# Kernel optimization log

Hardware: AMD Instinct MI355X
Metric: run time of the kernel (lower is better)

## Reference

```python
import jax, jax.numpy as jnp
import numpy as np

B, T, C, H = 2, 2048, 1024, 16
HS = C // H  # 64
EPS = 1e-5


def layer_norm(x, w, b):
    mu = jnp.mean(x, axis=-1, keepdims=True)
    var = jnp.var(x, axis=-1, keepdims=True)
    return (x - mu) * jax.lax.rsqrt(var + EPS) * w + b


def setup_inputs() -> dict:
    key = jax.random.key(0)
    ks = jax.random.split(key, 16)
    s_c = 1.0 / np.sqrt(C)
    s_f = 1.0 / np.sqrt(4 * C)
    u = lambda k, shape, s: jax.random.uniform(k, shape, jnp.float32, -s, s)
    return {
        "x": jax.random.normal(ks[0], (B, T, C), jnp.float32),
        # per-head Q/K/V Linears stacked over heads: [H, C, HS], bias [H, HS]
        "Wq": u(ks[1], (H, C, HS), s_c), "bq": u(ks[2], (H, HS), s_c),
        "Wk": u(ks[3], (H, C, HS), s_c), "bk": u(ks[4], (H, HS), s_c),
        "Wv": u(ks[5], (H, C, HS), s_c), "bv": u(ks[6], (H, HS), s_c),
        "Wp": u(ks[7], (C, C), s_c), "bp": u(ks[8], (C,), s_c),
        "W1": u(ks[9], (C, 4 * C), s_c), "b1": u(ks[10], (4 * C,), s_c),
        "W2": u(ks[11], (4 * C, C), s_f), "b2": u(ks[12], (C,), s_f),
        "ln1_w": jnp.ones((C,), jnp.float32), "ln1_b": jnp.zeros((C,), jnp.float32),
        "ln2_w": jnp.ones((C,), jnp.float32), "ln2_b": jnp.zeros((C,), jnp.float32),
    }


def reference(x, Wq, bq, Wk, bk, Wv, bv, Wp, bp, W1, b1, W2, b2,
              ln1_w, ln1_b, ln2_w, ln2_b):
    # --- pre-norm self-attention ---
    xn = layer_norm(x, ln1_w, ln1_b)
    q = jnp.einsum('btc,hcd->bhtd', xn, Wq) + bq[None, :, None, :]
    k = jnp.einsum('btc,hcd->bhtd', xn, Wk) + bk[None, :, None, :]
    v = jnp.einsum('btc,hcd->bhtd', xn, Wv) + bv[None, :, None, :]
    # NOTE: original scales by C**-0.5 (full embedding dim), not head_size**-0.5
    att = jnp.einsum('bhtd,bhsd->bhts', q, k) * (C ** -0.5)
    att = jax.nn.softmax(att, axis=-1)
    o = jnp.einsum('bhts,bhsd->bhtd', att, v)  # [B,H,T,HS]
    o = jnp.transpose(o, (0, 2, 1, 3)).reshape(B, T, C)  # concat heads
    sa = o @ Wp + bp
    out = x + sa
    # --- pre-norm FFN (exact erf GELU, matching nn.GELU default) ---
    on = layer_norm(out, ln2_w, ln2_b)
    h = jax.nn.gelu(on @ W1 + b1, approximate=False)
    return out + (h @ W2 + b2)
```

## Files before the change

### kernel.cpp

```cpp
#include <hip/hip_runtime.h>
#include <math.h>

#define BB 2
#define TT 2048
#define CC 1024
#define HH 16
#define HS 64
#define MT 4096
#define FF 4096

typedef unsigned short u16;
typedef __bf16 bfrag __attribute__((ext_vector_type(8)));
typedef float f4 __attribute__((ext_vector_type(4)));

#define AS1(p) ((const __attribute__((address_space(1))) void*)(p))
#define AS3(p) ((__attribute__((address_space(3))) void*)(p))

__device__ __forceinline__ u16 f2bf(float f) {
  union { float f; unsigned u; } a; a.f = f;
  return (u16)((a.u + 0x7fffu + ((a.u >> 16) & 1u)) >> 16);
}

__device__ __forceinline__ int swz128(int byteoff) {
  return byteoff ^ (((byteoff >> 7) & 7) << 4);
}

__global__ void tr_f32_bf16(const float* __restrict__ src, u16* __restrict__ dst,
                            int R, int Cc, long long sb, long long db, int dld) {
  __shared__ float t[32][33];
  const int bz = blockIdx.z;
  const int r0 = blockIdx.y * 32, c0 = blockIdx.x * 32;
  const int tx = threadIdx.x, ty = threadIdx.y;
  const float* s = src + bz * sb;
  u16* d = dst + bz * db;
#pragma unroll
  for (int i = 0; i < 4; i++)
    t[ty + i * 8][tx] = s[(size_t)(r0 + ty + i * 8) * Cc + c0 + tx];
  __syncthreads();
#pragma unroll
  for (int i = 0; i < 4; i++)
    d[(size_t)(c0 + ty + i * 8) * dld + r0 + tx] = f2bf(t[tx][ty + i * 8]);
}

__global__ void tr_bf16(const u16* __restrict__ src, u16* __restrict__ dst,
                        int R, int Cc, long long sb, long long db, int dld) {
  __shared__ u16 t[32][33];
  const int bz = blockIdx.z;
  const int r0 = blockIdx.y * 32, c0 = blockIdx.x * 32;
  const int tx = threadIdx.x, ty = threadIdx.y;
  const u16* s = src + bz * sb;
  u16* d = dst + bz * db;
#pragma unroll
  for (int i = 0; i < 4; i++)
    t[ty + i * 8][tx] = s[(size_t)(r0 + ty + i * 8) * Cc + c0 + tx];
  __syncthreads();
#pragma unroll
  for (int i = 0; i < 4; i++)
    d[(size_t)(c0 + ty + i * 8) * dld + r0 + tx] = t[tx][ty + i * 8];
}

__global__ __launch_bounds__(256) void ln_kernel(
    const float* __restrict__ x, const float* __restrict__ w,
    const float* __restrict__ b, u16* __restrict__ y) {
  const int row = blockIdx.x, tid = threadIdx.x;
  const float4 v = reinterpret_cast<const float4*>(x + (size_t)row * CC)[tid];
  float s = v.x + v.y + v.z + v.w;
  float s2 = v.x * v.x + v.y * v.y + v.z * v.z + v.w * v.w;
#pragma unroll
  for (int off = 32; off >= 1; off >>= 1) {
    s += __shfl_xor(s, off);
    s2 += __shfl_xor(s2, off);
  }
  __shared__ float ps[4], ps2[4];
  const int wave = tid >> 6, lane = tid & 63;
  if (lane == 0) { ps[wave] = s; ps2[wave] = s2; }
  __syncthreads();
  s = ps[0] + ps[1] + ps[2] + ps[3];
  s2 = ps2[0] + ps2[1] + ps2[2] + ps2[3];
  const float mu = s * (1.f / CC);
  const float rstd = rsqrtf(s2 * (1.f / CC) - mu * mu + 1e-5f);
  const float4 wv = reinterpret_cast<const float4*>(w)[tid];
  const float4 bv = reinterpret_cast<const float4*>(b)[tid];
  ushort4 o;
  o.x = f2bf((v.x - mu) * rstd * wv.x + bv.x);
  o.y = f2bf((v.y - mu) * rstd * wv.y + bv.y);
  o.z = f2bf((v.z - mu) * rstd * wv.z + bv.z);
  o.w = f2bf((v.w - mu) * rstd * wv.w + bv.w);
  reinterpret_cast<ushort4*>(y + (size_t)row * CC)[tid] = o;
}

__device__ __forceinline__ void gemm128_core(
    const u16* __restrict__ A, const u16* __restrict__ Bt, int K,
    f4 (&acc)[4][4]) {
  __shared__ u16 As[128 * 32];
  __shared__ u16 Bs[128 * 32];
  const int tid = threadIdx.x;
  const int wave = tid >> 6, lane = tid & 63;
  const int wm = wave >> 1, wn = wave & 1;
  const int lg = lane >> 4, ll = lane & 15;

  const u16* ga = A + (size_t)(blockIdx.y * 128 + (tid >> 2)) * K + (tid & 3) * 8;
  const u16* gb = Bt + (size_t)(blockIdx.x * 128 + (tid >> 2)) * K + (tid & 3) * 8;
  u16* la = As + tid * 8;
  u16* lb = Bs + tid * 8;
  const size_t g64 = (size_t)64 * K;

  for (int kt = 0; kt < K; kt += 32) {
    __builtin_amdgcn_global_load_lds(AS1(ga), AS3(la), 16, 0, 0);
    __builtin_amdgcn_global_load_lds(AS1(ga + g64), AS3(la + 2048), 16, 0, 0);
    __builtin_amdgcn_global_load_lds(AS1(gb), AS3(lb), 16, 0, 0);
    __builtin_amdgcn_global_load_lds(AS1(gb + g64), AS3(lb + 2048), 16, 0, 0);
    __syncthreads();
    bfrag af[4], bf[4];
#pragma unroll
    for (int i = 0; i < 4; i++) {
      af[i] = *(const bfrag*)&As[(wm * 64 + i * 16 + ll) * 32 + lg * 8];
      bf[i] = *(const bfrag*)&Bs[(wn * 64 + i * 16 + ll) * 32 + lg * 8];
    }
#pragma unroll
    for (int i = 0; i < 4; i++)
#pragma unroll
      for (int j = 0; j < 4; j++)
        acc[i][j] = __builtin_amdgcn_mfma_f32_16x16x32_bf16(af[i], bf[j], acc[i][j], 0, 0, 0);
    __syncthreads();
    ga += 32; gb += 32;
  }
}

#define EPI_COORDS                                              \
  const int tid = threadIdx.x;                                  \
  const int wave = tid >> 6, lane = tid & 63;                   \
  const int wm = wave >> 1, wn = wave & 1;                      \
  const int lg = lane >> 4, ll = lane & 15;

__global__ __launch_bounds__(256, 2) void gemm_qkv(
    const u16* __restrict__ A, const u16* __restrict__ Bt,
    const float* __restrict__ bq, const float* __restrict__ bk,
    const float* __restrict__ bv,
    u16* __restrict__ q, u16* __restrict__ k, u16* __restrict__ v) {
  f4 acc[4][4] = {};
  gemm128_core(A, Bt, CC, acc);
  EPI_COORDS
#pragma unroll
  for (int j = 0; j < 4; j++) {
    const int n = blockIdx.x * 128 + wn * 64 + j * 16 + ll;
    const int sec = n >> 10, nn = n & 1023, h = nn >> 6, d = nn & 63;
    const float bias = (sec == 0 ? bq : (sec == 1 ? bk : bv))[nn];
    const float scale = (sec == 0) ? 0.03125f : 1.0f;
    u16* dst = sec == 0 ? q : (sec == 1 ? k : v);
#pragma unroll
    for (int i = 0; i < 4; i++)
#pragma unroll
      for (int r = 0; r < 4; r++) {
        const int m = blockIdx.y * 128 + wm * 64 + i * 16 + lg * 4 + r;
        const int b = m >> 11, t = m & 2047;
        dst[(((size_t)b * HH + h) * TT + t) * HS + d] = f2bf((acc[i][j][r] + bias) * scale);
      }
  }
}

__global__ __launch_bounds__(256, 2) void gemm_proj(
    const u16* __restrict__ A, const u16* __restrict__ Bt,
    const float* __restrict__ bp, const float* __restrict__ x,
    float* __restrict__ outw) {
  f4 acc[4][4] = {};
  gemm128_core(A, Bt, CC, acc);
  EPI_COORDS
#pragma unroll
  for (int i = 0; i < 4; i++)
#pragma unroll
    for (int j = 0; j < 4; j++) {
      const int n = blockIdx.x * 128 + wn * 64 + j * 16 + ll;
      const float bias = bp[n];
#pragma unroll
      for (int r = 0; r < 4; r++) {
        const int m = blockIdx.y * 128 + wm * 64 + i * 16 + lg * 4 + r;
        const size_t idx = (size_t)m * CC + n;
        outw[idx] = acc[i][j][r] + bias + x[idx];
      }
    }
}

__global__ __launch_bounds__(256, 2) void gemm_ffn1(
    const u16* __restrict__ A, const u16* __restrict__ Bt,
    const float* __restrict__ b1, u16* __restrict__ hb) {
  f4 acc[4][4] = {};
  gemm128_core(A, Bt, CC, acc);
  EPI_COORDS
#pragma unroll
  for (int i = 0; i < 4; i++)
#pragma unroll
    for (int j = 0; j < 4; j++) {
      const int n = blockIdx.x * 128 + wn * 64 + j * 16 + ll;
      const float bias = b1[n];
#pragma unroll
      for (int r = 0; r < 4; r++) {
        const int m = blockIdx.y * 128 + wm * 64 + i * 16 + lg * 4 + r;
        const float t = acc[i][j][r] + bias;
        const float g = 0.5f * t * (1.0f + erff(t * 0.70710678118654752f));
        hb[(size_t)m * FF + n] = f2bf(g);
      }
    }
}

__global__ __launch_bounds__(256, 2) void gemm_ffn2(
    const u16* __restrict__ A, const u16* __restrict__ Bt,
    const float* __restrict__ b2, const float* __restrict__ outw,
    float* __restrict__ dout) {
  f4 acc[4][4] = {};
  gemm128_core(A, Bt, FF, acc);
  EPI_COORDS
#pragma unroll
  for (int i = 0; i < 4; i++)
#pragma unroll
    for (int j = 0; j < 4; j++) {
      const int n = blockIdx.x * 128 + wn * 64 + j * 16 + ll;
      const float bias = b2[n];
#pragma unroll
      for (int r = 0; r < 4; r++) {
        const int m = blockIdx.y * 128 + wm * 64 + i * 16 + lg * 4 + r;
        const size_t idx = (size_t)m * CC + n;
        dout[idx] = acc[i][j][r] + bias + outw[idx];
      }
    }
}

__global__ __launch_bounds__(256, 2) void attn_kernel(
    const u16* __restrict__ Q, const u16* __restrict__ Kb,
    const u16* __restrict__ Vt, u16* __restrict__ Ao) {
  __shared__ __align__(1024) u16 Ks[2][64 * 64];
  __shared__ __align__(1024) u16 Vs[2][64 * 64];
  __shared__ __align__(1024) u16 Ps[4][32 * 64];
  const int bh = blockIdx.y, qt = blockIdx.x;
  const int tid = threadIdx.x, wave = tid >> 6, lane = tid & 63;
  const int lg = lane >> 4, ll = lane & 15;

  bfrag qf[2][2];
  const u16* Qb = Q + ((size_t)bh * TT + qt * 128 + wave * 32) * HS;
#pragma unroll
  for (int qb = 0; qb < 2; qb++)
#pragma unroll
    for (int dc = 0; dc < 2; dc++)
      qf[qb][dc] = *(const bfrag*)&Qb[(qb * 16 + ll) * HS + dc * 32 + lg * 8];

  f4 o[2][4] = {};
  float mrun[2] = {-INFINITY, -INFINITY}, lrun[2] = {0.f, 0.f};

  const int trow = tid >> 3;
  const int tch  = (tid & 7) ^ (trow & 7);
  const u16* gk = Kb + ((size_t)bh * TT + trow) * HS + tch * 8;
  const u16* gv = Vt + ((size_t)bh * HS + trow) * TT + tch * 8;

  char* const pw = (char*)Ps[wave];

#define STAGE(bufi, stt)                                                          \
  do {                                                                            \
    u16* lk = &Ks[bufi][tid * 8];                                                 \
    u16* lv = &Vs[bufi][tid * 8];                                                 \
    __builtin_amdgcn_global_load_lds(AS1(gk + (size_t)(stt) * HS), AS3(lk), 16, 0, 0); \
    __builtin_amdgcn_global_load_lds(AS1(gk + (size_t)(stt) * HS + 32 * HS), AS3(lk + 2048), 16, 0, 0); \
    __builtin_amdgcn_global_load_lds(AS1(gv + (stt)), AS3(lv), 16, 0, 0);         \
    __builtin_amdgcn_global_load_lds(AS1(gv + (stt) + (size_t)32 * TT), AS3(lv + 2048), 16, 0, 0); \
  } while (0)

  STAGE(0, 0);
  int cur = 0;

  for (int st = 0; st < TT; st += 64) {
    if (st + 64 < TT) {
      STAGE(cur ^ 1, st + 64);
      asm volatile("s_waitcnt vmcnt(4)" ::: "memory");
    } else {
      asm volatile("s_waitcnt vmcnt(0)" ::: "memory");
    }
    __builtin_amdgcn_s_barrier();
    __builtin_amdgcn_sched_barrier(0);

    const char* kbuf = (const char*)Ks[cur];
    const char* vbuf = (const char*)Vs[cur];

    f4 p[2][4];
#pragma unroll
    for (int kb = 0; kb < 4; kb++) {
      const int row = kb * 16 + ll;
      const bfrag k0 = *(const bfrag*)(kbuf + swz128(row * 128 + lg * 16));
      const bfrag k1 = *(const bfrag*)(kbuf + swz128(row * 128 + 64 + lg * 16));
#pragma unroll
      for (int qb = 0; qb < 2; qb++) {
        f4 z = {0.f, 0.f, 0.f, 0.f};
        z = __builtin_amdgcn_mfma_f32_16x16x32_bf16(k0, qf[qb][0], z, 0, 0, 0);
        p[qb][kb] = __builtin_amdgcn_mfma_f32_16x16x32_bf16(k1, qf[qb][1], z, 0, 0, 0);
      }
    }

#pragma unroll
    for (int qb = 0; qb < 2; qb++) {
      float pm = p[qb][0][0];
#pragma unroll
      for (int kb = 0; kb < 4; kb++)
#pragma unroll
        for (int r = 0; r < 4; r++)
          if (kb | r) pm = fmaxf(pm, p[qb][kb][r]);
      pm = fmaxf(pm, __shfl_xor(pm, 16));
      pm = fmaxf(pm, __shfl_xor(pm, 32));
      const float mn = fmaxf(mrun[qb], pm);
      const float al = __expf(mrun[qb] - mn);
      mrun[qb] = mn;
      float rs = 0.f;
#pragma unroll
      for (int kb = 0; kb < 4; kb++)
#pragma unroll
        for (int r = 0; r < 4; r++) {
          const float e = __expf(p[qb][kb][r] - mn);
          p[qb][kb][r] = e;
          rs += e;
        }
      rs += __shfl_xor(rs, 16);
      rs += __shfl_xor(rs, 32);
      lrun[qb] = lrun[qb] * al + rs;
#pragma unroll
      for (int fo = 0; fo < 4; fo++) o[qb][fo] *= al;
#pragma unroll
      for (int kb = 0; kb < 4; kb++) {
        union { uint2 v; __bf16 h[4]; } w;
        w.h[0] = (__bf16)p[qb][kb][0];
        w.h[1] = (__bf16)p[qb][kb][1];
        w.h[2] = (__bf16)p[qb][kb][2];
        w.h[3] = (__bf16)p[qb][kb][3];
        *(uint2*)(pw + swz128((qb * 16 + ll) * 128 + kb * 32 + lg * 8)) = w.v;
      }
    }

#pragma unroll
    for (int ks = 0; ks < 2; ks++) {
      const bfrag pb0 = *(const bfrag*)(pw + swz128(ll * 128 + ks * 64 + lg * 16));
      const bfrag pb1 = *(const bfrag*)(pw + swz128((16 + ll) * 128 + ks * 64 + lg * 16));
#pragma unroll
      for (int fo = 0; fo < 4; fo++) {
        const bfrag vf = *(const bfrag*)(vbuf + swz128((fo * 16 + ll) * 128 + ks * 64 + lg * 16));
        o[0][fo] = __builtin_amdgcn_mfma_f32_16x16x32_bf16(vf, pb0, o[0][fo], 0, 0, 0);
        o[1][fo] = __builtin_amdgcn_mfma_f32_16x16x32_bf16(vf, pb1, o[1][fo], 0, 0, 0);
      }
    }

    __builtin_amdgcn_sched_barrier(0);
    __builtin_amdgcn_s_barrier();
    cur ^= 1;
  }
#undef STAGE

  const int b = bh >> 4, h = bh & 15;
#pragma unroll
  for (int qb = 0; qb < 2; qb++) {
    const float inv = 1.0f / lrun[qb];
    const int t = qt * 128 + wave * 32 + qb * 16 + ll;
#pragma unroll
    for (int fo = 0; fo < 4; fo++) {
      union { uint2 v; __bf16 h[4]; } w;
      w.h[0] = (__bf16)(o[qb][fo][0] * inv);
      w.h[1] = (__bf16)(o[qb][fo][1] * inv);
      w.h[2] = (__bf16)(o[qb][fo][2] * inv);
      w.h[3] = (__bf16)(o[qb][fo][3] * inv);
      *(uint2*)&Ao[((size_t)b * TT + t) * CC + h * HS + fo * 16 + lg * 4] = w.v;
    }
  }
}

extern "C" void kernel_launch(void* const* d_in, const int* in_sizes, int n_in,
                              void* d_out, int out_size, void* d_ws, size_t ws_size,
                              hipStream_t stream) {
  const float* x    = (const float*)d_in[0];
  const float* Wq   = (const float*)d_in[1];
  const float* bq   = (const float*)d_in[2];
  const float* Wk   = (const float*)d_in[3];
  const float* bk   = (const float*)d_in[4];
  const float* Wv   = (const float*)d_in[5];
  const float* bv   = (const float*)d_in[6];
  const float* Wp   = (const float*)d_in[7];
  const float* bp   = (const float*)d_in[8];
  const float* W1   = (const float*)d_in[9];
  const float* b1   = (const float*)d_in[10];
  const float* W2   = (const float*)d_in[11];
  const float* b2   = (const float*)d_in[12];
  const float* ln1w = (const float*)d_in[13];
  const float* ln1b = (const float*)d_in[14];
  const float* ln2w = (const float*)d_in[15];
  const float* ln2b = (const float*)d_in[16];
  float* dout = (float*)d_out;

  char* ws = (char*)d_ws;
  u16* wqkv = (u16*)(ws + 0);
  u16* wpt  = (u16*)(ws + 6291456);
  u16* w1t  = (u16*)(ws + 8388608);
  u16* w2t  = (u16*)(ws + 16777216);
  u16* xn   = (u16*)(ws + 25165824);
  u16* qb   = (u16*)(ws + 33554432);
  u16* kb   = (u16*)(ws + 41943040);
  u16* vb   = (u16*)(ws + 50331648);
  u16* vt   = (u16*)(ws + 58720256);
  u16* ao   = (u16*)(ws + 67108864);
  u16* hb   = qb;

  dim3 blk256(256);
  dim3 blkT(32, 8);

  tr_f32_bf16<<<dim3(2, 32, 16), blkT, 0, stream>>>(Wq, wqkv,               1024,   64, 65536LL, 65536LL, 1024);
  tr_f32_bf16<<<dim3(2, 32, 16), blkT, 0, stream>>>(Wk, wqkv + 1024 * 1024, 1024,   64, 65536LL, 65536LL, 1024);
  tr_f32_bf16<<<dim3(2, 32, 16), blkT, 0, stream>>>(Wv, wqkv + 2048 * 1024, 1024,   64, 65536LL, 65536LL, 1024);
  tr_f32_bf16<<<dim3(32, 32, 1),  blkT, 0, stream>>>(Wp, wpt, 1024, 1024, 0LL, 0LL, 1024);
  tr_f32_bf16<<<dim3(128, 32, 1), blkT, 0, stream>>>(W1, w1t, 1024, 4096, 0LL, 0LL, 1024);
  tr_f32_bf16<<<dim3(32, 128, 1), blkT, 0, stream>>>(W2, w2t, 4096, 1024, 0LL, 0LL, 4096);

  ln_kernel<<<dim3(MT), blk256, 0, stream>>>(x, ln1w, ln1b, xn);

  gemm_qkv<<<dim3(24, 32), blk256, 0, stream>>>(xn, wqkv, bq, bk, bv, qb, kb, vb);

  tr_bf16<<<dim3(2, 64, 32), blkT, 0, stream>>>(vb, vt, 2048, 64, 131072LL, 131072LL, 2048);

  attn_kernel<<<dim3(16, 32), blk256, 0, stream>>>(qb, kb, vt, ao);

  gemm_proj<<<dim3(8, 32), blk256, 0, stream>>>(ao, wpt, bp, x, dout);

  ln_kernel<<<dim3(MT), blk256, 0, stream>>>(dout, ln2w, ln2b, xn);

  gemm_ffn1<<<dim3(32, 32), blk256, 0, stream>>>(xn, w1t, b1, hb);
  gemm_ffn2<<<dim3(8, 32), blk256, 0, stream>>>(hb, w2t, b2, dout, dout);
}
```

Before: 298.0 us.

## Triple-buffer GEMM core with async LDS loads, swizzle, and narrower N tiles

Rewrites the shared GEMM core to use a 3-stage LDS ring fed by global_load_lds, with explicit vmcnt waits so loads for future k-tiles overlap MFMA work. An XOR swizzle on the 16-byte chunks is applied on the load and fragment-read sides to cut LDS bank conflicts, and MFMA sections raise wave priority. The proj and FFN2 GEMMs (N=1024) switch to 128x64 tiles so they launch twice as many blocks and fill the CUs better. The trade-off is roughly 3x the LDS per block, which may lower occupancy, plus hand-tuned waitcnt counts that must match the number of issued loads.

```diff
diff --git a/kernel.cpp b/kernel.cpp
--- a/kernel.cpp
+++ b/kernel.cpp
@@ -23,6 +23,10 @@
 
 __device__ __forceinline__ int swz128(int byteoff) {
   return byteoff ^ (((byteoff >> 7) & 7) << 4);
+}
+
+__device__ __forceinline__ int swzAB(int byteoff) {
+  return byteoff ^ (((byteoff >> 7) & 3) << 4);
 }
 
 __global__ void tr_f32_bf16(const float* __restrict__ src, u16* __restrict__ dst,
@@ -89,41 +93,77 @@
   reinterpret_cast<ushort4*>(y + (size_t)row * CC)[tid] = o;
 }
 
-__device__ __forceinline__ void gemm128_core(
+template<int NJ>
+__device__ __forceinline__ void gemm_core(
     const u16* __restrict__ A, const u16* __restrict__ Bt, int K,
-    f4 (&acc)[4][4]) {
-  __shared__ u16 As[128 * 32];
-  __shared__ u16 Bs[128 * 32];
+    f4 (&acc)[4][NJ]) {
+  constexpr int BN = NJ * 32;
+  __shared__ u16 As[3][128 * 32];
+  __shared__ u16 Bs[3][BN * 32];
   const int tid = threadIdx.x;
   const int wave = tid >> 6, lane = tid & 63;
   const int wm = wave >> 1, wn = wave & 1;
   const int lg = lane >> 4, ll = lane & 15;
 
-  const u16* ga = A + (size_t)(blockIdx.y * 128 + (tid >> 2)) * K + (tid & 3) * 8;
-  const u16* gb = Bt + (size_t)(blockIdx.x * 128 + (tid >> 2)) * K + (tid & 3) * 8;
-  u16* la = As + tid * 8;
-  u16* lb = Bs + tid * 8;
+  const int trow = tid >> 2;
+  const int tch  = (tid & 3) ^ ((trow >> 1) & 3);
+  const u16* ga = A + (size_t)(blockIdx.y * 128 + trow) * K + tch * 8;
+  const u16* gb = Bt + (size_t)(blockIdx.x * BN + trow) * K + tch * 8;
   const size_t g64 = (size_t)64 * K;
-
-  for (int kt = 0; kt < K; kt += 32) {
-    __builtin_amdgcn_global_load_lds(AS1(ga), AS3(la), 16, 0, 0);
-    __builtin_amdgcn_global_load_lds(AS1(ga + g64), AS3(la + 2048), 16, 0, 0);
-    __builtin_amdgcn_global_load_lds(AS1(gb), AS3(lb), 16, 0, 0);
-    __builtin_amdgcn_global_load_lds(AS1(gb + g64), AS3(lb + 2048), 16, 0, 0);
-    __syncthreads();
-    bfrag af[4], bf[4];
-#pragma unroll
-    for (int i = 0; i < 4; i++) {
-      af[i] = *(const bfrag*)&As[(wm * 64 + i * 16 + ll) * 32 + lg * 8];
-      bf[i] = *(const bfrag*)&Bs[(wn * 64 + i * 16 + ll) * 32 + lg * 8];
-    }
+  const int nt = K >> 5;
+
+  auto GSTAGE = [&](int bi, int kt) {
+    u16* la = &As[bi][tid * 8];
+    u16* lb = &Bs[bi][tid * 8];
+    const u16* gA = ga + kt * 32;
+    const u16* gB = gb + kt * 32;
+    __builtin_amdgcn_global_load_lds(AS1(gA), AS3(la), 16, 0, 0);
+    __builtin_amdgcn_global_load_lds(AS1(gA + g64), AS3(la + 2048), 16, 0, 0);
+    __builtin_amdgcn_global_load_lds(AS1(gB), AS3(lb), 16, 0, 0);
+    if constexpr (NJ == 4)
+      __builtin_amdgcn_global_load_lds(AS1(gB + g64), AS3(lb + 2048), 16, 0, 0);
+  };
+
+  GSTAGE(0, 0);
+  GSTAGE(1, 1);
+  GSTAGE(2, 2);
+  int bi = 0;
+  for (int t = 0; t < nt; t++) {
+    const int ahead = nt - 1 - t;
+    if constexpr (NJ == 4) {
+      if (ahead >= 2)      asm volatile("s_waitcnt vmcnt(8)" ::: "memory");
+      else if (ahead == 1) asm volatile("s_waitcnt vmcnt(4)" ::: "memory");
+      else                 asm volatile("s_waitcnt vmcnt(0)" ::: "memory");
+    } else {
+      if (ahead >= 2)      asm volatile("s_waitcnt vmcnt(6)" ::: "memory");
+      else if (ahead == 1) asm volatile("s_waitcnt vmcnt(3)" ::: "memory");
+      else                 asm volatile("s_waitcnt vmcnt(0)" ::: "memory");
+    }
+    __builtin_amdgcn_s_barrier();
+    __builtin_amdgcn_sched_barrier(0);
+
+    const char* as_ = (const char*)As[bi];
+    const char* bs_ = (const char*)Bs[bi];
+    bfrag af[4], bf[NJ];
 #pragma unroll
     for (int i = 0; i < 4; i++)
-#pragma unroll
-      for (int j = 0; j < 4; j++)
+      af[i] = *(const bfrag*)(as_ + swzAB((wm * 64 + i * 16 + ll) * 64 + lg * 16));
+#pragma unroll
+    for (int j = 0; j < NJ; j++)
+      bf[j] = *(const bfrag*)(bs_ + swzAB((wn * (BN / 2) + j * 16 + ll) * 64 + lg * 16));
+
+    __builtin_amdgcn_s_setprio(1);
+#pragma unroll
+    for (int i = 0; i < 4; i++)
+#pragma unroll
+      for (int j = 0; j < NJ; j++)
         acc[i][j] = __builtin_amdgcn_mfma_f32_16x16x32_bf16(af[i], bf[j], acc[i][j], 0, 0, 0);
-    __syncthreads();
-    ga += 32; gb += 32;
+    __builtin_amdgcn_s_setprio(0);
+
+    __builtin_amdgcn_sched_barrier(0);
+    __builtin_amdgcn_s_barrier();
+    if (t + 3 < nt) GSTAGE(bi, t + 3);
+    bi = (bi == 2) ? 0 : bi + 1;
   }
 }
 
@@ -139,7 +179,7 @@
     const float* __restrict__ bv,
     u16* __restrict__ q, u16* __restrict__ k, u16* __restrict__ v) {
   f4 acc[4][4] = {};
-  gemm128_core(A, Bt, CC, acc);
+  gemm_core<4>(A, Bt, CC, acc);
   EPI_COORDS
 #pragma unroll
   for (int j = 0; j < 4; j++) {
@@ -163,14 +203,14 @@
     const u16* __restrict__ A, const u16* __restrict__ Bt,
     const float* __restrict__ bp, const float* __restrict__ x,
     float* __restrict__ outw) {
-  f4 acc[4][4] = {};
-  gemm128_core(A, Bt, CC, acc);
+  f4 acc[4][2] = {};
+  gemm_core<2>(A, Bt, CC, acc);
   EPI_COORDS
 #pragma unroll
   for (int i = 0; i < 4; i++)
 #pragma unroll
-    for (int j = 0; j < 4; j++) {
-      const int n = blockIdx.x * 128 + wn * 64 + j * 16 + ll;
+    for (int j = 0; j < 2; j++) {
+      const int n = blockIdx.x * 64 + wn * 32 + j * 16 + ll;
       const float bias = bp[n];
 #pragma unroll
       for (int r = 0; r < 4; r++) {
@@ -185,7 +225,7 @@
     const u16* __restrict__ A, const u16* __restrict__ Bt,
     const float* __restrict__ b1, u16* __restrict__ hb) {
   f4 acc[4][4] = {};
-  gemm128_core(A, Bt, CC, acc);
+  gemm_core<4>(A, Bt, CC, acc);
   EPI_COORDS
 #pragma unroll
   for (int i = 0; i < 4; i++)
@@ -207,14 +247,14 @@
     const u16* __restrict__ A, const u16* __restrict__ Bt,
     const float* __restrict__ b2, const float* __restrict__ outw,
     float* __restrict__ dout) {
-  f4 acc[4][4] = {};
-  gemm128_core(A, Bt, FF, acc);
+  f4 acc[4][2] = {};
+  gemm_core<2>(A, Bt, FF, acc);
   EPI_COORDS
 #pragma unroll
   for (int i = 0; i < 4; i++)
 #pragma unroll
-    for (int j = 0; j < 4; j++) {
-      const int n = blockIdx.x * 128 + wn * 64 + j * 16 + ll;
+    for (int j = 0; j < 2; j++) {
+      const int n = blockIdx.x * 64 + wn * 32 + j * 16 + ll;
       const float bias = b2[n];
 #pragma unroll
       for (int r = 0; r < 4; r++) {
@@ -419,10 +459,10 @@
 
   attn_kernel<<<dim3(16, 32), blk256, 0, stream>>>(qb, kb, vt, ao);
 
-  gemm_proj<<<dim3(8, 32), blk256, 0, stream>>>(ao, wpt, bp, x, dout);
+  gemm_proj<<<dim3(16, 32), blk256, 0, stream>>>(ao, wpt, bp, x, dout);
 
   ln_kernel<<<dim3(MT), blk256, 0, stream>>>(dout, ln2w, ln2b, xn);
 
   gemm_ffn1<<<dim3(32, 32), blk256, 0, stream>>>(xn, w1t, b1, hb);
-  gemm_ffn2<<<dim3(8, 32), blk256, 0, stream>>>(hb, w2t, b2, dout, dout);
-}
+  gemm_ffn2<<<dim3(16, 32), blk256, 0, stream>>>(hb, w2t, b2, dout, dout);
+}
```

New measurement: 292.0 us. 2.0% less time.
